# Kernel optimization log

Hardware: AMD Instinct MI355X
Metric: run time of the kernel (lower is better)

The kernel has to match this reference:

```python
import jax, jax.numpy as jnp
import numpy as np

EPS = 1e-8  # torch CosineSimilarity eps


def _cosine_sim_matrix(x, y):
    # x: [Nx, D], y: [Ny, D] -> [Nx, Ny] cosine similarity via normalized GEMM
    xn = x / jnp.maximum(jnp.linalg.norm(x, axis=-1, keepdims=True), EPS)
    yn = y / jnp.maximum(jnp.linalg.norm(y, axis=-1, keepdims=True), EPS)
    return xn @ yn.T


def setup_inputs() -> dict:
    key = jax.random.key(0)
    k1, k2, k3, k4 = jax.random.split(key, 4)
    N, D, C = 4096, 512, 100
    inst_embed = jax.random.normal(k1, (N, D), dtype=jnp.float32)
    proxy = jax.random.normal(k2, (N, D), dtype=jnp.float32)
    # binary positive-selection mask per class over the batch
    negative_mask = (jax.random.uniform(k3, (C, N)) > 0.5).astype(jnp.float32)
    labels = jax.random.randint(k4, (N,), 0, C, dtype=jnp.int64)
    temperature = jnp.float32(0.1)
    margin = jnp.float32(0.0)
    return {"inst_embed": inst_embed, "proxy": proxy,
            "negative_mask": negative_mask, "labels": labels,
            "temperature": temperature, "margin": margin}


def reference(inst_embed, proxy, negative_mask, labels, temperature, margin):
    # [N, N] similarity matrices
    p2i = _cosine_sim_matrix(proxy, inst_embed)
    i2i = _cosine_sim_matrix(inst_embed, inst_embed)
    p2i_zone = jnp.exp((p2i - margin) / temperature)
    i2i_zone = jnp.exp((i2i - margin) / temperature)
    mask = negative_mask[labels]  # [N, N]
    p2i_num = (p2i_zone * mask).sum(axis=1)
    i2i_num = (i2i_zone * mask).sum(axis=1)
    p2i_den = p2i_zone.sum(axis=1)
    i2i_den = i2i_zone.sum(axis=1)
    p2i_loss = -jnp.log(temperature * (p2i_num / p2i_den)).mean()
    i2i_loss = -jnp.log(temperature * (i2i_num / i2i_den)).mean()
    return p2i_loss + i2i_loss
```

## Files before the change

kernel.cpp:

```cpp
#include <hip/hip_runtime.h>
#include <hip/hip_bf16.h>

#define D_DIM 512
#define KSTEPS 16
#define BM 64
#define BN 32
#define GRIDY 8

typedef __bf16 bf16x8 __attribute__((ext_vector_type(8)));
typedef float  f32x4  __attribute__((ext_vector_type(4)));

__device__ __forceinline__ unsigned short f2bf_rne(float x) {
    unsigned int u = __float_as_uint(x);
    u += 0x7FFFu + ((u >> 16) & 1u);
    return (unsigned short)(u >> 16);
}

__device__ __forceinline__ void g2l16(const void* g, void* l) {
    __builtin_amdgcn_global_load_lds(
        (const __attribute__((address_space(1))) unsigned int*)g,
        (__attribute__((address_space(3))) unsigned int*)l, 16, 0, 0);
}

__global__ __launch_bounds__(256) void normalize_rows(
    const float* __restrict__ inst, const float* __restrict__ proxy,
    unsigned short* __restrict__ instb, unsigned short* __restrict__ proxyb,
    float* __restrict__ nd, int N)
{
    const int lane = threadIdx.x & 63;
    const int wave = threadIdx.x >> 6;
    const int base = blockIdx.x * 16 + wave * 4;
    #pragma unroll
    for (int i = 0; i < 4; ++i) {
        const int row = base + i;
        const float* src;
        unsigned short* dst;
        if (row < N) { src = inst  + (size_t)row * D_DIM;        dst = instb  + (size_t)row * D_DIM; }
        else         { src = proxy + (size_t)(row - N) * D_DIM;  dst = proxyb + (size_t)(row - N) * D_DIM; }
        float4 v0 = ((const float4*)src)[lane * 2];
        float4 v1 = ((const float4*)src)[lane * 2 + 1];
        float ss = v0.x*v0.x + v0.y*v0.y + v0.z*v0.z + v0.w*v0.w
                 + v1.x*v1.x + v1.y*v1.y + v1.z*v1.z + v1.w*v1.w;
        #pragma unroll
        for (int off = 32; off > 0; off >>= 1) ss += __shfl_xor(ss, off, 64);
        const float inv = 1.0f / fmaxf(sqrtf(ss), 1e-8f);
        ushort4 o0, o1;
        o0.x = f2bf_rne(v0.x * inv); o0.y = f2bf_rne(v0.y * inv);
        o0.z = f2bf_rne(v0.z * inv); o0.w = f2bf_rne(v0.w * inv);
        o1.x = f2bf_rne(v1.x * inv); o1.y = f2bf_rne(v1.y * inv);
        o1.z = f2bf_rne(v1.z * inv); o1.w = f2bf_rne(v1.w * inv);
        ((ushort4*)dst)[lane * 2]     = o0;
        ((ushort4*)dst)[lane * 2 + 1] = o1;
    }
    if (blockIdx.x < 16)
        ((float4*)nd)[blockIdx.x * 256 + threadIdx.x] = make_float4(0.f, 0.f, 0.f, 0.f);
}

__global__ __launch_bounds__(256, 2) void fused_scores(
    const unsigned short* __restrict__ instb,
    const unsigned short* __restrict__ proxyb,
    const float* __restrict__ negmask,
    const int*  __restrict__ labels,
    const float* __restrict__ temp_p,
    const float* __restrict__ margin_p,
    float* __restrict__ nd,
    int N, int colsPerBlock)
{
    __shared__ unsigned short Bt0[BN * D_DIM];
    __shared__ unsigned short Bt1[BN * D_DIM];

    const int tid  = threadIdx.x;
    const int lane = tid & 63;
    const int wave = tid >> 6;
    const int quad = lane >> 4;
    const int l16  = lane & 15;

    const int row0 = blockIdx.x * BM + wave * 16;

    const float temp  = *temp_p;
    const float scale = 1.44269504088896340736f / temp;
    const float bias  = -(*margin_p) * scale;

    bf16x8 Ap[KSTEPS], Ai[KSTEPS];
    {
        const unsigned short* pr = proxyb + (size_t)(row0 + l16) * D_DIM + quad * 8;
        const unsigned short* ir = instb  + (size_t)(row0 + l16) * D_DIM + quad * 8;
        #pragma unroll
        for (int ks = 0; ks < KSTEPS; ks++) {
            Ap[ks] = *(const bf16x8*)(pr + ks * 32);
            Ai[ks] = *(const bf16x8*)(ir + ks * 32);
        }
    }

    int lab[4];
    #pragma unroll
    for (int r = 0; r < 4; r++) lab[r] = labels[row0 + quad * 4 + r];

    float numP[4] = {0.f,0.f,0.f,0.f}, denP[4] = {0.f,0.f,0.f,0.f};
    float numI[4] = {0.f,0.f,0.f,0.f}, denI[4] = {0.f,0.f,0.f,0.f};

    const int j0base = blockIdx.y * colsPerBlock;
    const int nt     = colsPerBlock / BN;

    auto stage = [&](unsigned short (&B)[BN * D_DIM], int t) {
        const int j0 = j0base + t * BN;
        #pragma unroll
        for (int it = 0; it < BN / 4; ++it) {
            const int br = it * 4 + wave;
            const unsigned short* src =
                instb + (size_t)(j0 + br) * D_DIM + ((lane ^ (br & 7)) * 8);
            g2l16(src, &B[br * D_DIM]);
        }
    };

    auto compute = [&](unsigned short (&B)[BN * D_DIM], int t) {
        const int j0 = j0base + t * BN;
        f32x4 accP[2] = {}, accI[2] = {};
        #pragma unroll
        for (int ks = 0; ks < KSTEPS; ++ks) {
            #pragma unroll
            for (int cg = 0; cg < 2; ++cg) {
                const int rB  = cg * 16 + l16;
                const int chs = (ks * 4 + quad) ^ (rB & 7);
                bf16x8 b = *(const bf16x8*)&B[(size_t)rB * D_DIM + chs * 8];
                accP[cg] = __builtin_amdgcn_mfma_f32_16x16x32_bf16(Ap[ks], b, accP[cg], 0, 0, 0);
                accI[cg] = __builtin_amdgcn_mfma_f32_16x16x32_bf16(Ai[ks], b, accI[cg], 0, 0, 0);
            }
        }
        #pragma unroll
        for (int cg = 0; cg < 2; ++cg) {
            const int j = j0 + cg * 16 + l16;
            #pragma unroll
            for (int r = 0; r < 4; ++r) {
                const float m = negmask[(size_t)lab[r] * N + j];
                float zp = exp2f(accP[cg][r] * scale + bias);
                float zi = exp2f(accI[cg][r] * scale + bias);
                denP[r] += zp; numP[r] += zp * m;
                denI[r] += zi; numI[r] += zi * m;
            }
        }
    };

    stage(Bt0, 0);
    __syncthreads();
    for (int t = 0; t < nt; t += 2) {
        stage(Bt1, t + 1);
        compute(Bt0, t);
        __syncthreads();
        if (t + 2 < nt) stage(Bt0, t + 2);
        compute(Bt1, t + 1);
        __syncthreads();
    }

    #pragma unroll
    for (int r = 0; r < 4; r++) {
        float np = numP[r], dp = denP[r], ni = numI[r], di = denI[r];
        #pragma unroll
        for (int off = 8; off > 0; off >>= 1) {
            np += __shfl_down(np, off, 16);
            dp += __shfl_down(dp, off, 16);
            ni += __shfl_down(ni, off, 16);
            di += __shfl_down(di, off, 16);
        }
        if (l16 == 0) {
            const int row = row0 + quad * 4 + r;
            atomicAdd(&nd[row],         np);
            atomicAdd(&nd[N + row],     dp);
            atomicAdd(&nd[2 * N + row], ni);
            atomicAdd(&nd[3 * N + row], di);
        }
    }
}

__global__ __launch_bounds__(1024) void loss_reduce(
    const float* __restrict__ nd, const float* __restrict__ temp_p,
    float* __restrict__ out, int N)
{
    const float t = *temp_p;
    float s = 0.f;
    for (int i = threadIdx.x; i < N; i += 1024) {
        s += (logf(nd[N + i])     - logf(nd[i]));
        s += (logf(nd[3 * N + i]) - logf(nd[2 * N + i]));
    }
    #pragma unroll
    for (int off = 32; off > 0; off >>= 1) s += __shfl_down(s, off, 64);
    __shared__ float wss[16];
    if ((threadIdx.x & 63) == 0) wss[threadIdx.x >> 6] = s;
    __syncthreads();
    if (threadIdx.x < 16) {
        float v = wss[threadIdx.x];
        #pragma unroll
        for (int off = 8; off > 0; off >>= 1) v += __shfl_down(v, off, 16);
        if (threadIdx.x == 0) out[0] = v / (float)N - 2.0f * logf(t);
    }
}

extern "C" void kernel_launch(void* const* d_in, const int* in_sizes, int n_in,
                              void* d_out, int out_size, void* d_ws, size_t ws_size,
                              hipStream_t stream)
{
    const float* inst     = (const float*)d_in[0];
    const float* proxy    = (const float*)d_in[1];
    const float* negmask  = (const float*)d_in[2];
    const int*   labels   = (const int*)d_in[3];
    const float* temp_p   = (const float*)d_in[4];
    const float* margin_p = (const float*)d_in[5];
    float* out = (float*)d_out;

    const int N = in_sizes[3];

    unsigned short* instb  = (unsigned short*)d_ws;
    unsigned short* proxyb = instb + (size_t)N * D_DIM;
    float* nd = (float*)(proxyb + (size_t)N * D_DIM);

    normalize_rows<<<2 * N / 16, 256, 0, stream>>>(inst, proxy, instb, proxyb, nd, N);
    dim3 grid(N / BM, GRIDY);
    fused_scores<<<grid, 256, 0, stream>>>(instb, proxyb, negmask, labels,
                                           temp_p, margin_p, nd, N, N / GRIDY);
    loss_reduce<<<1, 1024, 0, stream>>>(nd, temp_p, out, N);
}
```

Before: 119.9 us.

## Double rows per wave to reuse each B fragment across four MFMAs

Each wave now computes 32 rows instead of 16, holding two sets of A fragments in registers so every LDS-loaded B fragment feeds four MFMAs instead of two. Mask values are also prefetched before the MFMA loop so their global-load latency overlaps the matrix work. The aim is to halve LDS reads per MFMA and cut the block count. In exchange register pressure doubles (64 bf16x8 A fragments), occupancy drops to one block per CU, and there are half as many blocks in the grid.

```diff
diff --git a/kernel.cpp b/kernel.cpp
--- a/kernel.cpp
+++ b/kernel.cpp
@@ -3,7 +3,7 @@
 
 #define D_DIM 512
 #define KSTEPS 16
-#define BM 64
+#define BM 128
 #define BN 32
 #define GRIDY 8
 
@@ -56,7 +56,7 @@
         ((float4*)nd)[blockIdx.x * 256 + threadIdx.x] = make_float4(0.f, 0.f, 0.f, 0.f);
 }
 
-__global__ __launch_bounds__(256, 2) void fused_scores(
+__global__ __launch_bounds__(256, 1) void fused_scores(
     const unsigned short* __restrict__ instb,
     const unsigned short* __restrict__ proxyb,
     const float* __restrict__ negmask,
@@ -75,29 +75,36 @@
     const int quad = lane >> 4;
     const int l16  = lane & 15;
 
-    const int row0 = blockIdx.x * BM + wave * 16;
+    const int row0 = blockIdx.x * BM + wave * 32;
 
     const float temp  = *temp_p;
     const float scale = 1.44269504088896340736f / temp;
     const float bias  = -(*margin_p) * scale;
 
-    bf16x8 Ap[KSTEPS], Ai[KSTEPS];
+    bf16x8 Ap0[KSTEPS], Ai0[KSTEPS], Ap1[KSTEPS], Ai1[KSTEPS];
     {
-        const unsigned short* pr = proxyb + (size_t)(row0 + l16) * D_DIM + quad * 8;
-        const unsigned short* ir = instb  + (size_t)(row0 + l16) * D_DIM + quad * 8;
+        const unsigned short* p0 = proxyb + (size_t)(row0 + l16)      * D_DIM + quad * 8;
+        const unsigned short* i0 = instb  + (size_t)(row0 + l16)      * D_DIM + quad * 8;
+        const unsigned short* p1 = proxyb + (size_t)(row0 + 16 + l16) * D_DIM + quad * 8;
+        const unsigned short* i1 = instb  + (size_t)(row0 + 16 + l16) * D_DIM + quad * 8;
         #pragma unroll
         for (int ks = 0; ks < KSTEPS; ks++) {
-            Ap[ks] = *(const bf16x8*)(pr + ks * 32);
-            Ai[ks] = *(const bf16x8*)(ir + ks * 32);
-        }
-    }
-
-    int lab[4];
-    #pragma unroll
-    for (int r = 0; r < 4; r++) lab[r] = labels[row0 + quad * 4 + r];
-
-    float numP[4] = {0.f,0.f,0.f,0.f}, denP[4] = {0.f,0.f,0.f,0.f};
-    float numI[4] = {0.f,0.f,0.f,0.f}, denI[4] = {0.f,0.f,0.f,0.f};
+            Ap0[ks] = *(const bf16x8*)(p0 + ks * 32);
+            Ai0[ks] = *(const bf16x8*)(i0 + ks * 32);
+            Ap1[ks] = *(const bf16x8*)(p1 + ks * 32);
+            Ai1[ks] = *(const bf16x8*)(i1 + ks * 32);
+        }
+    }
+
+    int lab[2][4];
+    #pragma unroll
+    for (int g = 0; g < 2; g++)
+        #pragma unroll
+        for (int r = 0; r < 4; r++)
+            lab[g][r] = labels[row0 + g * 16 + quad * 4 + r];
+
+    float numP[2][4] = {}, denP[2][4] = {};
+    float numI[2][4] = {}, denI[2][4] = {};
 
     const int j0base = blockIdx.y * colsPerBlock;
     const int nt     = colsPerBlock / BN;
@@ -115,7 +122,16 @@
 
     auto compute = [&](unsigned short (&B)[BN * D_DIM], int t) {
         const int j0 = j0base + t * BN;
-        f32x4 accP[2] = {}, accI[2] = {};
+        float mk[2][2][4];
+        #pragma unroll
+        for (int g = 0; g < 2; ++g)
+            #pragma unroll
+            for (int c = 0; c < 2; ++c)
+                #pragma unroll
+                for (int r = 0; r < 4; ++r)
+                    mk[g][c][r] = negmask[(size_t)lab[g][r] * N + (j0 + c * 16 + l16)];
+
+        f32x4 aP0[2] = {}, aI0[2] = {}, aP1[2] = {}, aI1[2] = {};
         #pragma unroll
         for (int ks = 0; ks < KSTEPS; ++ks) {
             #pragma unroll
@@ -123,20 +139,25 @@
                 const int rB  = cg * 16 + l16;
                 const int chs = (ks * 4 + quad) ^ (rB & 7);
                 bf16x8 b = *(const bf16x8*)&B[(size_t)rB * D_DIM + chs * 8];
-                accP[cg] = __builtin_amdgcn_mfma_f32_16x16x32_bf16(Ap[ks], b, accP[cg], 0, 0, 0);
-                accI[cg] = __builtin_amdgcn_mfma_f32_16x16x32_bf16(Ai[ks], b, accI[cg], 0, 0, 0);
-            }
-        }
+                aP0[cg] = __builtin_amdgcn_mfma_f32_16x16x32_bf16(Ap0[ks], b, aP0[cg], 0, 0, 0);
+                aI0[cg] = __builtin_amdgcn_mfma_f32_16x16x32_bf16(Ai0[ks], b, aI0[cg], 0, 0, 0);
+                aP1[cg] = __builtin_amdgcn_mfma_f32_16x16x32_bf16(Ap1[ks], b, aP1[cg], 0, 0, 0);
+                aI1[cg] = __builtin_amdgcn_mfma_f32_16x16x32_bf16(Ai1[ks], b, aI1[cg], 0, 0, 0);
+            }
+        }
+
         #pragma unroll
         for (int cg = 0; cg < 2; ++cg) {
-            const int j = j0 + cg * 16 + l16;
             #pragma unroll
             for (int r = 0; r < 4; ++r) {
-                const float m = negmask[(size_t)lab[r] * N + j];
-                float zp = exp2f(accP[cg][r] * scale + bias);
-                float zi = exp2f(accI[cg][r] * scale + bias);
-                denP[r] += zp; numP[r] += zp * m;
-                denI[r] += zi; numI[r] += zi * m;
+                float zp0 = exp2f(aP0[cg][r] * scale + bias);
+                float zi0 = exp2f(aI0[cg][r] * scale + bias);
+                float zp1 = exp2f(aP1[cg][r] * scale + bias);
+                float zi1 = exp2f(aI1[cg][r] * scale + bias);
+                denP[0][r] += zp0; numP[0][r] += zp0 * mk[0][cg][r];
+                denI[0][r] += zi0; numI[0][r] += zi0 * mk[0][cg][r];
+                denP[1][r] += zp1; numP[1][r] += zp1 * mk[1][cg][r];
+                denI[1][r] += zi1; numI[1][r] += zi1 * mk[1][cg][r];
             }
         }
     };
@@ -153,21 +174,24 @@
     }
 
     #pragma unroll
-    for (int r = 0; r < 4; r++) {
-        float np = numP[r], dp = denP[r], ni = numI[r], di = denI[r];
-        #pragma unroll
-        for (int off = 8; off > 0; off >>= 1) {
-            np += __shfl_down(np, off, 16);
-            dp += __shfl_down(dp, off, 16);
-            ni += __shfl_down(ni, off, 16);
-            di += __shfl_down(di, off, 16);
-        }
-        if (l16 == 0) {
-            const int row = row0 + quad * 4 + r;
-            atomicAdd(&nd[row],         np);
-            atomicAdd(&nd[N + row],     dp);
-            atomicAdd(&nd[2 * N + row], ni);
-            atomicAdd(&nd[3 * N + row], di);
+    for (int g = 0; g < 2; ++g) {
+        #pragma unroll
+        for (int r = 0; r < 4; ++r) {
+            float np = numP[g][r], dp = denP[g][r], ni = numI[g][r], di = denI[g][r];
+            #pragma unroll
+            for (int off = 8; off > 0; off >>= 1) {
+                np += __shfl_down(np, off, 16);
+                dp += __shfl_down(dp, off, 16);
+                ni += __shfl_down(ni, off, 16);
+                di += __shfl_down(di, off, 16);
+            }
+            if (l16 == 0) {
+                const int row = row0 + g * 16 + quad * 4 + r;
+                atomicAdd(&nd[row],         np);
+                atomicAdd(&nd[N + row],     dp);
+                atomicAdd(&nd[2 * N + row], ni);
+                atomicAdd(&nd[3 * N + row], di);
+            }
         }
     }
 }
```

After: 129.5 us. 8.0% more time.

## Fuse loss reduction into scores kernel via last-block counter; single-buffer wider B tile

Applied to the files above, without the earlier changes.

Removes the separate loss_reduce launch: a global counter, reset by normalize_rows, lets the last block of fused_scores compute the final log-sum loss. The B tile widens from 32 to 64 columns and the LDS double buffer becomes a single buffer with two barriers per tile, so global-to-LDS loads no longer overlap the MFMA work. This saves one launch and halves the number of tile iterations, but exposes load latency and leaves the whole final reduction to one 256-thread block.

```diff
diff --git a/kernel.cpp b/kernel.cpp
--- a/kernel.cpp
+++ b/kernel.cpp
@@ -4,7 +4,7 @@
 #define D_DIM 512
 #define KSTEPS 16
 #define BM 64
-#define BN 32
+#define BN 64
 #define GRIDY 8
 
 typedef __bf16 bf16x8 __attribute__((ext_vector_type(8)));
@@ -25,7 +25,7 @@
 __global__ __launch_bounds__(256) void normalize_rows(
     const float* __restrict__ inst, const float* __restrict__ proxy,
     unsigned short* __restrict__ instb, unsigned short* __restrict__ proxyb,
-    float* __restrict__ nd, int N)
+    float* __restrict__ nd, int* __restrict__ ctr, int N)
 {
     const int lane = threadIdx.x & 63;
     const int wave = threadIdx.x >> 6;
@@ -54,6 +54,7 @@
     }
     if (blockIdx.x < 16)
         ((float4*)nd)[blockIdx.x * 256 + threadIdx.x] = make_float4(0.f, 0.f, 0.f, 0.f);
+    if (blockIdx.x == 16 && threadIdx.x == 0) *ctr = 0;
 }
 
 __global__ __launch_bounds__(256, 2) void fused_scores(
@@ -64,10 +65,11 @@
     const float* __restrict__ temp_p,
     const float* __restrict__ margin_p,
     float* __restrict__ nd,
+    int* __restrict__ ctr,
+    float* __restrict__ out,
     int N, int colsPerBlock)
 {
-    __shared__ unsigned short Bt0[BN * D_DIM];
-    __shared__ unsigned short Bt1[BN * D_DIM];
+    __shared__ unsigned short Bt[BN * D_DIM];
 
     const int tid  = threadIdx.x;
     const int lane = tid & 63;
@@ -100,35 +102,33 @@
     float numI[4] = {0.f,0.f,0.f,0.f}, denI[4] = {0.f,0.f,0.f,0.f};
 
     const int j0base = blockIdx.y * colsPerBlock;
-    const int nt     = colsPerBlock / BN;
-
-    auto stage = [&](unsigned short (&B)[BN * D_DIM], int t) {
-        const int j0 = j0base + t * BN;
-        #pragma unroll
-        for (int it = 0; it < BN / 4; ++it) {
+    for (int jt = 0; jt < colsPerBlock; jt += BN) {
+        const int j0 = j0base + jt;
+        __syncthreads();
+        #pragma unroll
+        for (int it = 0; it < (BN * (D_DIM / 8)) / 256; it++) {
             const int br = it * 4 + wave;
             const unsigned short* src =
                 instb + (size_t)(j0 + br) * D_DIM + ((lane ^ (br & 7)) * 8);
-            g2l16(src, &B[br * D_DIM]);
-        }
-    };
-
-    auto compute = [&](unsigned short (&B)[BN * D_DIM], int t) {
-        const int j0 = j0base + t * BN;
-        f32x4 accP[2] = {}, accI[2] = {};
+            g2l16(src, &Bt[(size_t)br * D_DIM]);
+        }
+        __syncthreads();
+
+        f32x4 accP[4] = {}, accI[4] = {};
         #pragma unroll
         for (int ks = 0; ks < KSTEPS; ++ks) {
             #pragma unroll
-            for (int cg = 0; cg < 2; ++cg) {
+            for (int cg = 0; cg < 4; ++cg) {
                 const int rB  = cg * 16 + l16;
                 const int chs = (ks * 4 + quad) ^ (rB & 7);
-                bf16x8 b = *(const bf16x8*)&B[(size_t)rB * D_DIM + chs * 8];
+                bf16x8 b = *(const bf16x8*)&Bt[(size_t)rB * D_DIM + chs * 8];
                 accP[cg] = __builtin_amdgcn_mfma_f32_16x16x32_bf16(Ap[ks], b, accP[cg], 0, 0, 0);
                 accI[cg] = __builtin_amdgcn_mfma_f32_16x16x32_bf16(Ai[ks], b, accI[cg], 0, 0, 0);
             }
         }
-        #pragma unroll
-        for (int cg = 0; cg < 2; ++cg) {
+
+        #pragma unroll
+        for (int cg = 0; cg < 4; ++cg) {
             const int j = j0 + cg * 16 + l16;
             #pragma unroll
             for (int r = 0; r < 4; ++r) {
@@ -139,17 +139,6 @@
                 denI[r] += zi; numI[r] += zi * m;
             }
         }
-    };
-
-    stage(Bt0, 0);
-    __syncthreads();
-    for (int t = 0; t < nt; t += 2) {
-        stage(Bt1, t + 1);
-        compute(Bt0, t);
-        __syncthreads();
-        if (t + 2 < nt) stage(Bt0, t + 2);
-        compute(Bt1, t + 1);
-        __syncthreads();
     }
 
     #pragma unroll
@@ -170,28 +159,33 @@
             atomicAdd(&nd[3 * N + row], di);
         }
     }
-}
-
-__global__ __launch_bounds__(1024) void loss_reduce(
-    const float* __restrict__ nd, const float* __restrict__ temp_p,
-    float* __restrict__ out, int N)
-{
-    const float t = *temp_p;
-    float s = 0.f;
-    for (int i = threadIdx.x; i < N; i += 1024) {
-        s += (logf(nd[N + i])     - logf(nd[i]));
-        s += (logf(nd[3 * N + i]) - logf(nd[2 * N + i]));
-    }
-    #pragma unroll
-    for (int off = 32; off > 0; off >>= 1) s += __shfl_down(s, off, 64);
-    __shared__ float wss[16];
-    if ((threadIdx.x & 63) == 0) wss[threadIdx.x >> 6] = s;
+
+    __shared__ int isLast;
+    __threadfence();
+    if (tid == 0) {
+        int prev = __hip_atomic_fetch_add(ctr, 1, __ATOMIC_ACQ_REL,
+                                          __HIP_MEMORY_SCOPE_AGENT);
+        isLast = (prev == (int)(gridDim.x * gridDim.y) - 1);
+    }
     __syncthreads();
-    if (threadIdx.x < 16) {
-        float v = wss[threadIdx.x];
-        #pragma unroll
-        for (int off = 8; off > 0; off >>= 1) v += __shfl_down(v, off, 16);
-        if (threadIdx.x == 0) out[0] = v / (float)N - 2.0f * logf(t);
+    if (isLast) {
+        float s = 0.f;
+        for (int i = tid; i < N; i += 256) {
+            float pn  = __hip_atomic_load(&nd[i],         __ATOMIC_RELAXED, __HIP_MEMORY_SCOPE_AGENT);
+            float pd  = __hip_atomic_load(&nd[N + i],     __ATOMIC_RELAXED, __HIP_MEMORY_SCOPE_AGENT);
+            float in_ = __hip_atomic_load(&nd[2 * N + i], __ATOMIC_RELAXED, __HIP_MEMORY_SCOPE_AGENT);
+            float id  = __hip_atomic_load(&nd[3 * N + i], __ATOMIC_RELAXED, __HIP_MEMORY_SCOPE_AGENT);
+            s += (logf(pd) - logf(pn)) + (logf(id) - logf(in_));
+        }
+        #pragma unroll
+        for (int off = 32; off > 0; off >>= 1) s += __shfl_down(s, off, 64);
+        float* wss = (float*)Bt;
+        __syncthreads();
+        if ((tid & 63) == 0) wss[tid >> 6] = s;
+        __syncthreads();
+        if (tid == 0)
+            out[0] = (wss[0] + wss[1] + wss[2] + wss[3]) / (float)N
+                   - 2.0f * logf(temp);
     }
 }
 
@@ -212,10 +206,12 @@
     unsigned short* instb  = (unsigned short*)d_ws;
     unsigned short* proxyb = instb + (size_t)N * D_DIM;
     float* nd = (float*)(proxyb + (size_t)N * D_DIM);
-
-    normalize_rows<<<2 * N / 16, 256, 0, stream>>>(inst, proxy, instb, proxyb, nd, N);
+    int*  ctr = (int*)(nd + 4 * (size_t)N);
+
+    normalize_rows<<<2 * N / 16, 256, 0, stream>>>(inst, proxy, instb, proxyb,
+                                                   nd, ctr, N);
     dim3 grid(N / BM, GRIDY);
     fused_scores<<<grid, 256, 0, stream>>>(instb, proxyb, negmask, labels,
-                                           temp_p, margin_p, nd, N, N / GRIDY);
-    loss_reduce<<<1, 1024, 0, stream>>>(nd, temp_p, out, N);
-}
+                                           temp_p, margin_p, nd, ctr, out,
+                                           N, N / GRIDY);
+}
```

Measured after the change: 164.6 us. 37.2% more time.
